# Kernel optimization log

Measured on AMD Instinct MI355X. Metric: run time of the kernel, lower is better.

Reference implementation:

```python
import jax, jax.numpy as jnp
import numpy as np

NQ = 14
DIM = 2 ** NQ


def make_unitary(M):
    # QR-based unitarization, matching torch: Q * (diag(R)/|diag(R)|) broadcast over rows
    Q, R = jnp.linalg.qr(M)
    d = jnp.diagonal(R, axis1=-2, axis2=-1)
    ph = d / jnp.abs(d)
    return Q * ph[..., None, :]


def apply_1q(state, U, q, nq):
    # state: [B] + [2]*nq, qubit q lives at axis 1 + (nq-1-q) (qubit 0 = LSB)
    ax = 1 + (nq - 1 - q)
    s = jnp.moveaxis(state, ax, 1)
    shp = s.shape
    s = s.reshape(shp[0], 2, -1)
    s = jnp.einsum('ji,bir->bjr', U, s)
    return jnp.moveaxis(s.reshape(shp), 1, ax)


def apply_1q_batched(state, U, q, nq):
    # U: [B,2,2] per-batch gate
    ax = 1 + (nq - 1 - q)
    s = jnp.moveaxis(state, ax, 1)
    shp = s.shape
    s = s.reshape(shp[0], 2, -1)
    s = jnp.einsum('bji,bir->bjr', U, s)
    return jnp.moveaxis(s.reshape(shp), 1, ax)


def apply_2q(state, U4, qa, qb, nq):
    # source: gate index = bit_qa + 2*bit_qb, so reshape(4,4)->(2,2,2,2) gives [ob,oa,ib,ia]
    G = U4.reshape(2, 2, 2, 2)
    ax_a = 1 + (nq - 1 - qa)
    ax_b = 1 + (nq - 1 - qb)
    s = jnp.moveaxis(state, (ax_b, ax_a), (1, 2))
    shp = s.shape
    s = s.reshape(shp[0], 2, 2, -1)
    s = jnp.einsum('JKjk,bjkr->bJKr', G, s)
    return jnp.moveaxis(s.reshape(shp), (1, 2), (ax_b, ax_a))


def setup_inputs() -> dict:
    key = jax.random.key(0)
    ks = jax.random.split(key, 9)
    B, H = 256, 1024
    return {
        'x': jax.random.normal(ks[0], (B, H), dtype=jnp.float32),
        'w_pre': jax.random.normal(ks[1], (2 * NQ, H), dtype=jnp.float32) * 0.03,
        'b_pre': jax.random.normal(ks[2], (2 * NQ,), dtype=jnp.float32) * 0.01,
        'w_post': jax.random.normal(ks[3], (H, DIM), dtype=jnp.float32) * 0.01,
        'b_post': jax.random.normal(ks[4], (H,), dtype=jnp.float32) * 0.01,
        'sq_re': jax.random.normal(ks[5], (NQ, 2, 2), dtype=jnp.float32),
        'sq_im': jax.random.normal(ks[6], (NQ, 2, 2), dtype=jnp.float32),
        'ent_re': jax.random.normal(ks[7], (NQ - 1, 4, 4), dtype=jnp.float32),
        'ent_im': jax.random.normal(ks[8], (NQ - 1, 4, 4), dtype=jnp.float32),
    }


def reference(x, w_pre, b_pre, w_post, b_post, sq_re, sq_im, ent_re, ent_im):
    B = x.shape[0]
    nq = NQ
    # pre_quantum Linear
    params = x @ w_pre.T + b_pre  # [B, 2*nq]
    theta = params[:, 0::2]
    phi = params[:, 1::2]
    c = jnp.cos(theta / 2)
    s = jnp.sin(theta / 2)
    # initial state = rotation gates applied to |0...0>: keep only column 0 of each gate
    v = jnp.stack([c.astype(jnp.complex64), (jnp.exp(1j * phi) * s).astype(jnp.complex64)], axis=-1)  # [B,nq,2]
    state = v[:, nq - 1]  # MSB axis first (qubit nq-1)
    for q in range(nq - 2, -1, -1):
        state = (state[:, :, None] * v[:, q][:, None, :]).reshape(B, -1)
    state = state.reshape((B,) + (2,) * nq)
    # learned unitaries (batched QR over gate index)
    sq = make_unitary(sq_re.astype(jnp.complex64) + 1j * sq_im.astype(jnp.complex64))
    ent = make_unitary(ent_re.astype(jnp.complex64) + 1j * ent_im.astype(jnp.complex64))
    for q in range(nq):
        state = apply_1q(state, sq[q], q, nq)
    for q in range(nq - 1):
        state = apply_2q(state, ent[q], q, q + 1, nq)
    amp = state.reshape(B, -1)  # C-order flatten => index = sum(bit_q << q), matches source
    probs = amp.real ** 2 + amp.imag ** 2  # [B, dim]
    return probs @ w_post.T + b_post  # [B, hidden]
```

## Files before the change

### kernel.cpp

```cpp
#include <hip/hip_runtime.h>
#include <hip/hip_bf16.h>
#include <math.h>

#define NQ 14
#define DIM 16384
#define NB 256
#define NH 1024
#define SPLITK 16
#define KCHUNK (DIM / SPLITK)
#define BK 64

typedef __attribute__((ext_vector_type(8))) short bf16x8;
typedef __attribute__((ext_vector_type(4))) float f32x4;

#define SW(i) ((i) + 5 * ((i) >> 5))
#define SW_SIZE (DIM + 5 * (DIM / 32))

__global__ __launch_bounds__(256) void k_pre(const float* __restrict__ x,
                                             const float* __restrict__ w_pre,
                                             const float* __restrict__ b_pre,
                                             float* __restrict__ v_buf) {
    int b = blockIdx.x;
    int t = threadIdx.x;
    __shared__ float red[28][4];

    float4 xs = ((const float4*)(x + (size_t)b * NH))[t];
    float acc[28];
#pragma unroll
    for (int j = 0; j < 28; j++) {
        float4 w = ((const float4*)(w_pre + (size_t)j * NH))[t];
        acc[j] = xs.x * w.x + xs.y * w.y + xs.z * w.z + xs.w * w.w;
    }
    int lane = t & 63, wv = t >> 6;
#pragma unroll
    for (int j = 0; j < 28; j++) {
        float a = acc[j];
#pragma unroll
        for (int o = 32; o > 0; o >>= 1) a += __shfl_down(a, o);
        if (lane == 0) red[j][wv] = a;
    }
    __syncthreads();
    if (t < NQ) {
        float p0 = red[2*t][0] + red[2*t][1] + red[2*t][2] + red[2*t][3] + b_pre[2*t];
        float p1 = red[2*t+1][0] + red[2*t+1][1] + red[2*t+1][2] + red[2*t+1][3] + b_pre[2*t+1];
        float c = cosf(p0 * 0.5f), s = sinf(p0 * 0.5f);
        float cp = cosf(p1), sp = sinf(p1);
        ((float4*)v_buf)[b * NQ + t] = make_float4(c, 0.f, cp * s, sp * s);
    }
}

template <int N>
__device__ void gs_qr(const float* Mre, const float* Mim, float* Uout) {
    double qre[N][N], qim[N][N];
#pragma unroll
    for (int j = 0; j < N; j++) {
        double vr[N], vi[N];
#pragma unroll
        for (int r = 0; r < N; r++) { vr[r] = (double)Mre[r * N + j]; vi[r] = (double)Mim[r * N + j]; }
#pragma unroll
        for (int i = 0; i < N; i++) {
            if (i < j) {
                double rr = 0.0, ri = 0.0;
#pragma unroll
                for (int r = 0; r < N; r++) {
                    rr += qre[i][r] * vr[r] + qim[i][r] * vi[r];
                    ri += qre[i][r] * vi[r] - qim[i][r] * vr[r];
                }
#pragma unroll
                for (int r = 0; r < N; r++) {
                    vr[r] -= rr * qre[i][r] - ri * qim[i][r];
                    vi[r] -= rr * qim[i][r] + ri * qre[i][r];
                }
            }
        }
        double nn = 0.0;
#pragma unroll
        for (int r = 0; r < N; r++) nn += vr[r] * vr[r] + vi[r] * vi[r];
        double inv = 1.0 / sqrt(nn);
#pragma unroll
        for (int r = 0; r < N; r++) { qre[j][r] = vr[r] * inv; qim[j][r] = vi[r] * inv; }
    }
#pragma unroll
    for (int r = 0; r < N; r++)
#pragma unroll
        for (int j = 0; j < N; j++) {
            Uout[(r * N + j) * 2]     = (float)qre[j][r];
            Uout[(r * N + j) * 2 + 1] = (float)qim[j][r];
        }
}

__global__ void k_qr(const float* __restrict__ sq_re, const float* __restrict__ sq_im,
                     const float* __restrict__ ent_re, const float* __restrict__ ent_im,
                     float* __restrict__ sqU, float* __restrict__ entU) {
    int t = threadIdx.x;
    if (t < NQ) {
        gs_qr<2>(sq_re + t * 4, sq_im + t * 4, sqU + t * 8);
    } else if (t < NQ + (NQ - 1)) {
        int e = t - NQ;
        gs_qr<4>(ent_re + e * 16, ent_im + e * 16, entU + e * 32);
    }
}

extern __shared__ float smem[];
__global__ __launch_bounds__(1024) void k_state(const float* __restrict__ v_buf,
                                                const float* __restrict__ sqU,
                                                const float* __restrict__ entU,
                                                __hip_bfloat16* __restrict__ probs) {
    const int b = blockIdx.x, t = threadIdx.x;
    float* sre  = smem;
    float* simg = smem + SW_SIZE;
    float* wloc = smem + 2 * SW_SIZE;
    float* g2   = wloc + NQ * 4;
    float* hi   = g2 + (NQ - 1) * 32;

    if (t < (NQ - 1) * 32) g2[t] = entU[t];
    if (t < NQ) {
        float4 v = ((const float4*)v_buf)[b * NQ + t];
        const float* u = sqU + t * 8;
        float w0r = u[0]*v.x - u[1]*v.y + u[2]*v.z - u[3]*v.w;
        float w0i = u[0]*v.y + u[1]*v.x + u[2]*v.w + u[3]*v.z;
        float w1r = u[4]*v.x - u[5]*v.y + u[6]*v.z - u[7]*v.w;
        float w1i = u[4]*v.y + u[5]*v.x + u[6]*v.w + u[7]*v.z;
        wloc[t*4+0] = w0r; wloc[t*4+1] = w0i; wloc[t*4+2] = w1r; wloc[t*4+3] = w1i;
    }
    __syncthreads();
    if (t < 16) {
        float hr = 1.f, hii = 0.f;
#pragma unroll
        for (int q = 10; q < 14; q++) {
            int bit = (t >> (q - 10)) & 1;
            float br = wloc[q*4 + 2*bit], bi = wloc[q*4 + 2*bit + 1];
            float nr = hr*br - hii*bi, ni = hr*bi + hii*br;
            hr = nr; hii = ni;
        }
        hi[2*t] = hr; hi[2*t+1] = hii;
    }
    __syncthreads();
    {
        float lr = 1.f, li = 0.f;
#pragma unroll
        for (int q = 0; q < 10; q++) {
            int bit = (t >> q) & 1;
            float br = wloc[q*4 + 2*bit], bi = wloc[q*4 + 2*bit + 1];
            float nr = lr*br - li*bi, ni = lr*bi + li*br;
            lr = nr; li = ni;
        }
#pragma unroll
        for (int k = 0; k < 16; k++) {
            int idx = k * 1024 + t;
            float hr = hi[2*k], hii = hi[2*k+1];
            sre[SW(idx)]  = lr*hr - li*hii;
            simg[SW(idx)] = lr*hii + li*hr;
        }
    }
    __syncthreads();

    for (int e = 0; e < NQ - 1; e++) {
        float gr[4][4], gi[4][4];
#pragma unroll
        for (int m = 0; m < 16; m++) {
            gr[m >> 2][m & 3] = g2[e*32 + 2*m];
            gi[m >> 2][m & 3] = g2[e*32 + 2*m + 1];
        }
        const int q = e, mask = (1 << q) - 1;
#pragma unroll
        for (int k = 0; k < 4; k++) {
            int g = k * 1024 + t;
            int base = ((g & ~mask) << 2) | (g & mask);
            int ia[4];
#pragma unroll
            for (int m = 0; m < 4; m++) ia[m] = SW(base + (m << q));
            float ar[4], ai[4];
#pragma unroll
            for (int m = 0; m < 4; m++) { ar[m] = sre[ia[m]]; ai[m] = simg[ia[m]]; }
            float orr[4], oii[4];
#pragma unroll
            for (int r = 0; r < 4; r++) {
                float nr = 0.f, ni = 0.f;
#pragma unroll
                for (int c = 0; c < 4; c++) {
                    nr += gr[r][c] * ar[c] - gi[r][c] * ai[c];
                    ni += gr[r][c] * ai[c] + gi[r][c] * ar[c];
                }
                orr[r] = nr; oii[r] = ni;
            }
#pragma unroll
            for (int r = 0; r < 4; r++) { sre[ia[r]] = orr[r]; simg[ia[r]] = oii[r]; }
        }
        __syncthreads();
    }

#pragma unroll
    for (int k = 0; k < 16; k++) {
        int idx = k * 1024 + t;
        float r = sre[SW(idx)], i2 = simg[SW(idx)];
        probs[(size_t)b * DIM + idx] = __float2bfloat16(r * r + i2 * i2);
    }
}

__global__ __launch_bounds__(512) void k_gemm_mfma(const ushort* __restrict__ A,
                                                   const float* __restrict__ Bw,
                                                   float* __restrict__ part) {
    __shared__ ushort As[128 * 64];
    __shared__ ushort Bs[128 * 64];
    const int t = threadIdx.x;
    const int l = t & 63, wid = t >> 6;
    const int wr = wid >> 2, wc = wid & 3;
    const int bm0 = blockIdx.x * 128;
    const int hn0 = blockIdx.y * 128;
    const int k0  = blockIdx.z * KCHUNK;

    f32x4 acc[4][2];
#pragma unroll
    for (int m = 0; m < 4; m++)
#pragma unroll
        for (int n = 0; n < 2; n++) acc[m][n] = (f32x4){0.f, 0.f, 0.f, 0.f};

    const int srow = t >> 3;
    const int scol = (t & 7) * 8;
    const int alr  = l >> 3;
    const int alc  = (l & 7) * 8;

    for (int kc = 0; kc < KCHUNK; kc += BK) {
        const int kbase = k0 + kc;
#pragma unroll
        for (int i = 0; i < 2; i++) {
            const int r0 = i * 64 + wid * 8;
            const ushort* gsrc = A + (size_t)(bm0 + r0 + alr) * DIM + kbase + alc;
            __builtin_amdgcn_global_load_lds(
                (const __attribute__((address_space(1))) unsigned int*)gsrc,
                (__attribute__((address_space(3))) unsigned int*)&As[r0 * 64],
                16, 0, 0);
        }
#pragma unroll
        for (int i = 0; i < 2; i++) {
            const int r = i * 64 + srow;
            const float* bsrc = Bw + (size_t)(hn0 + r) * DIM + kbase + scol;
            float4 b0 = *(const float4*)(bsrc);
            float4 b1 = *(const float4*)(bsrc + 4);
            union { ushort u[8]; bf16x8 v; } pk;
            __hip_bfloat16 h;
            h = __float2bfloat16(b0.x); pk.u[0] = *(ushort*)&h;
            h = __float2bfloat16(b0.y); pk.u[1] = *(ushort*)&h;
            h = __float2bfloat16(b0.z); pk.u[2] = *(ushort*)&h;
            h = __float2bfloat16(b0.w); pk.u[3] = *(ushort*)&h;
            h = __float2bfloat16(b1.x); pk.u[4] = *(ushort*)&h;
            h = __float2bfloat16(b1.y); pk.u[5] = *(ushort*)&h;
            h = __float2bfloat16(b1.z); pk.u[6] = *(ushort*)&h;
            h = __float2bfloat16(b1.w); pk.u[7] = *(ushort*)&h;
            *(bf16x8*)&Bs[r * 64 + scol] = pk.v;
        }
        __syncthreads();
#pragma unroll
        for (int kk = 0; kk < 2; kk++) {
            const int kcol = kk * 32 + (l >> 4) * 8;
            bf16x8 a[4], b[2];
#pragma unroll
            for (int m = 0; m < 4; m++)
                a[m] = *(const bf16x8*)&As[(wr * 64 + m * 16 + (l & 15)) * 64 + kcol];
#pragma unroll
            for (int n = 0; n < 2; n++)
                b[n] = *(const bf16x8*)&Bs[(wc * 32 + n * 16 + (l & 15)) * 64 + kcol];
#pragma unroll
            for (int m = 0; m < 4; m++)
#pragma unroll
                for (int n = 0; n < 2; n++)
                    acc[m][n] = __builtin_amdgcn_mfma_f32_16x16x32_bf16(
                        a[m], b[n], acc[m][n], 0, 0, 0);
        }
        __syncthreads();
    }
    float* dst = part + (size_t)blockIdx.z * (NB * NH);
#pragma unroll
    for (int m = 0; m < 4; m++) {
        const int row = bm0 + wr * 64 + m * 16 + (l >> 4) * 4;
#pragma unroll
        for (int n = 0; n < 2; n++) {
            const int col = hn0 + wc * 32 + n * 16 + (l & 15);
#pragma unroll
            for (int j = 0; j < 4; j++)
                dst[(size_t)(row + j) * NH + col] = acc[m][n][j];
        }
    }
}

__global__ __launch_bounds__(256) void k_reduce(const float* __restrict__ part,
                                                const float* __restrict__ b_post,
                                                float* __restrict__ out) {
    int i = blockIdx.x * 256 + threadIdx.x;
    float s = b_post[i & (NH - 1)];
#pragma unroll
    for (int z = 0; z < SPLITK; z++) s += part[(size_t)z * (NB * NH) + i];
    out[i] = s;
}

extern "C" void kernel_launch(void* const* d_in, const int* in_sizes, int n_in,
                              void* d_out, int out_size, void* d_ws, size_t ws_size,
                              hipStream_t stream) {
    const float* x      = (const float*)d_in[0];
    const float* w_pre  = (const float*)d_in[1];
    const float* b_pre  = (const float*)d_in[2];
    const float* w_post = (const float*)d_in[3];
    const float* b_post = (const float*)d_in[4];
    const float* sq_re  = (const float*)d_in[5];
    const float* sq_im  = (const float*)d_in[6];
    const float* ent_re = (const float*)d_in[7];
    const float* ent_im = (const float*)d_in[8];
    float* out = (float*)d_out;
    char* ws   = (char*)d_ws;

    float* v_buf         = (float*)(ws);
    float* sqU           = (float*)(ws + 57344);
    float* entU          = (float*)(ws + 57792);
    __hip_bfloat16* probs = (__hip_bfloat16*)(ws + 59456);
    float* part          = (float*)(ws + 8448064);

    k_pre<<<NB, 256, 0, stream>>>(x, w_pre, b_pre, v_buf);
    k_qr<<<1, 64, 0, stream>>>(sq_re, sq_im, ent_re, ent_im, sqU, entU);

    const int smem_bytes = (2 * SW_SIZE + NQ * 4 + (NQ - 1) * 32 + 32) * 4;
    (void)hipFuncSetAttribute((const void*)k_state,
                              hipFuncAttributeMaxDynamicSharedMemorySize, smem_bytes);
    k_state<<<NB, 1024, smem_bytes, stream>>>(v_buf, sqU, entU, probs);

    k_gemm_mfma<<<dim3(2, 8, SPLITK), 512, 0, stream>>>((const ushort*)probs, w_post, part);
    k_reduce<<<(NB * NH) / 256, 256, 0, stream>>>(part, b_post, out);
}
```

Measured before the change: 206.5 us.

## Register-resident gate chain with shared-memory transposes, fuse QR into pre kernel, smaller GEMM tiles

The state kernel now keeps 16 amplitudes per thread in registers and applies three 2-qubit gates locally between shared-memory transposes. This replaces a per-gate shared-memory round trip plus barrier for each of the 13 gates. The QR kernel launch is folded into extra blocks of the pre kernel to save one launch. The GEMM switches to 64x64 tiles with 256 threads, giving more blocks for occupancy at the cost of lower per-block data reuse.

```diff
diff --git a/kernel.cpp b/kernel.cpp
--- a/kernel.cpp
+++ b/kernel.cpp
@@ -16,12 +16,66 @@
 #define SW(i) ((i) + 5 * ((i) >> 5))
 #define SW_SIZE (DIM + 5 * (DIM / 32))
 
+template <int N>
+__device__ void gs_qr(const float* Mre, const float* Mim, float* Uout) {
+    double qre[N][N], qim[N][N];
+#pragma unroll
+    for (int j = 0; j < N; j++) {
+        double vr[N], vi[N];
+#pragma unroll
+        for (int r = 0; r < N; r++) { vr[r] = (double)Mre[r * N + j]; vi[r] = (double)Mim[r * N + j]; }
+#pragma unroll
+        for (int i = 0; i < N; i++) {
+            if (i < j) {
+                double rr = 0.0, ri = 0.0;
+#pragma unroll
+                for (int r = 0; r < N; r++) {
+                    rr += qre[i][r] * vr[r] + qim[i][r] * vi[r];
+                    ri += qre[i][r] * vi[r] - qim[i][r] * vr[r];
+                }
+#pragma unroll
+                for (int r = 0; r < N; r++) {
+                    vr[r] -= rr * qre[i][r] - ri * qim[i][r];
+                    vi[r] -= rr * qim[i][r] + ri * qre[i][r];
+                }
+            }
+        }
+        double nn = 0.0;
+#pragma unroll
+        for (int r = 0; r < N; r++) nn += vr[r] * vr[r] + vi[r] * vi[r];
+        double inv = 1.0 / sqrt(nn);
+#pragma unroll
+        for (int r = 0; r < N; r++) { qre[j][r] = vr[r] * inv; qim[j][r] = vi[r] * inv; }
+    }
+#pragma unroll
+    for (int r = 0; r < N; r++)
+#pragma unroll
+        for (int j = 0; j < N; j++) {
+            Uout[(r * N + j) * 2]     = (float)qre[j][r];
+            Uout[(r * N + j) * 2 + 1] = (float)qim[j][r];
+        }
+}
+
 __global__ __launch_bounds__(256) void k_pre(const float* __restrict__ x,
                                              const float* __restrict__ w_pre,
                                              const float* __restrict__ b_pre,
-                                             float* __restrict__ v_buf) {
-    int b = blockIdx.x;
-    int t = threadIdx.x;
+                                             const float* __restrict__ sq_re,
+                                             const float* __restrict__ sq_im,
+                                             const float* __restrict__ ent_re,
+                                             const float* __restrict__ ent_im,
+                                             float* __restrict__ v_buf,
+                                             float* __restrict__ sqU,
+                                             float* __restrict__ entU) {
+    const int b = blockIdx.x;
+    const int t = threadIdx.x;
+    if (b >= NB) {
+        if (b == NB) {
+            if (t < NQ) gs_qr<2>(sq_re + t * 4, sq_im + t * 4, sqU + t * 8);
+        } else {
+            if (t < NQ - 1) gs_qr<4>(ent_re + t * 16, ent_im + t * 16, entU + t * 32);
+        }
+        return;
+    }
     __shared__ float red[28][4];
 
     float4 xs = ((const float4*)(x + (size_t)b * NH))[t];
@@ -49,57 +103,48 @@
     }
 }
 
-template <int N>
-__device__ void gs_qr(const float* Mre, const float* Mim, float* Uout) {
-    double qre[N][N], qim[N][N];
-#pragma unroll
-    for (int j = 0; j < N; j++) {
-        double vr[N], vi[N];
-#pragma unroll
-        for (int r = 0; r < N; r++) { vr[r] = (double)Mre[r * N + j]; vi[r] = (double)Mim[r * N + j]; }
-#pragma unroll
-        for (int i = 0; i < N; i++) {
-            if (i < j) {
-                double rr = 0.0, ri = 0.0;
-#pragma unroll
-                for (int r = 0; r < N; r++) {
-                    rr += qre[i][r] * vr[r] + qim[i][r] * vi[r];
-                    ri += qre[i][r] * vi[r] - qim[i][r] * vr[r];
-                }
-#pragma unroll
-                for (int r = 0; r < N; r++) {
-                    vr[r] -= rr * qre[i][r] - ri * qim[i][r];
-                    vi[r] -= rr * qim[i][r] + ri * qre[i][r];
-                }
-            }
-        }
-        double nn = 0.0;
-#pragma unroll
-        for (int r = 0; r < N; r++) nn += vr[r] * vr[r] + vi[r] * vi[r];
-        double inv = 1.0 / sqrt(nn);
-#pragma unroll
-        for (int r = 0; r < N; r++) { qre[j][r] = vr[r] * inv; qim[j][r] = vi[r] * inv; }
-    }
-#pragma unroll
-    for (int r = 0; r < N; r++)
-#pragma unroll
-        for (int j = 0; j < N; j++) {
-            Uout[(r * N + j) * 2]     = (float)qre[j][r];
-            Uout[(r * N + j) * 2 + 1] = (float)qim[j][r];
-        }
-}
-
-__global__ void k_qr(const float* __restrict__ sq_re, const float* __restrict__ sq_im,
-                     const float* __restrict__ ent_re, const float* __restrict__ ent_im,
-                     float* __restrict__ sqU, float* __restrict__ entU) {
-    int t = threadIdx.x;
-    if (t < NQ) {
-        gs_qr<2>(sq_re + t * 4, sq_im + t * 4, sqU + t * 8);
-    } else if (t < NQ + (NQ - 1)) {
-        int e = t - NQ;
-        gs_qr<4>(ent_re + e * 16, ent_im + e * 16, entU + e * 32);
-    }
-}
+#define APPLY_GATE(I, GP) do {                                                \
+    float gr_[16], gi_[16];                                                   \
+    _Pragma("unroll")                                                         \
+    for (int m_ = 0; m_ < 16; m_++) { gr_[m_] = (GP)[2*m_]; gi_[m_] = (GP)[2*m_+1]; } \
+    _Pragma("unroll")                                                         \
+    for (int g_ = 0; g_ < 4; g_++) {                                          \
+        const int base_ = (I)==0 ? (g_<<2) : ((I)==1 ? ((g_&1)|((g_>>1)<<3)) : g_); \
+        float xr_[4], xi_[4];                                                 \
+        _Pragma("unroll")                                                     \
+        for (int c_ = 0; c_ < 4; c_++) { xr_[c_] = ar[base_+(c_<<(I))]; xi_[c_] = ai[base_+(c_<<(I))]; } \
+        _Pragma("unroll")                                                     \
+        for (int r_ = 0; r_ < 4; r_++) {                                      \
+            float nr_ = 0.f, ni_ = 0.f;                                       \
+            _Pragma("unroll")                                                 \
+            for (int c_ = 0; c_ < 4; c_++) {                                  \
+                nr_ += gr_[r_*4+c_]*xr_[c_] - gi_[r_*4+c_]*xi_[c_];           \
+                ni_ += gr_[r_*4+c_]*xi_[c_] + gi_[r_*4+c_]*xr_[c_];           \
+            }                                                                 \
+            ar[base_+(r_<<(I))] = nr_; ai[base_+(r_<<(I))] = ni_;             \
+        }                                                                     \
+    }                                                                         \
+} while (0)
+
+#define IDX_W0(r) (((t) << 4) | (r))
+#define IDX_W1(r) (((t) & 7) | ((r) << 3) | (((t) >> 3) << 7))
+#define IDX_W2(r) (((t) & 63) | ((r) << 6) | (((t) >> 6) << 10))
+#define IDX_W3(r) (((t) & 511) | ((r) << 9) | (((t) >> 9) << 13))
+#define IDX_W4(r) ((t) | ((r) << 10))
+
+#define TRANSPOSE(IDX_OLD, IDX_NEW) do {                                      \
+    _Pragma("unroll")                                                         \
+    for (int r_ = 0; r_ < 16; r_++) {                                         \
+        int o_ = SW(IDX_OLD(r_));                                             \
+        sre[o_] = ar[r_]; simg[o_] = ai[r_];                                  \
+    }                                                                         \
+    __syncthreads();                                                          \
+    _Pragma("unroll")                                                         \
+    for (int r_ = 0; r_ < 16; r_++) {                                         \
+        int n_ = SW(IDX_NEW(r_));                                             \
+        ar[r_] = sre[n_]; ai[r_] = simg[n_];                                  \
+    }                                                                         \
+} while (0)
 
 extern __shared__ float smem[];
 __global__ __launch_bounds__(1024) void k_state(const float* __restrict__ v_buf,
@@ -111,7 +156,6 @@
     float* simg = smem + SW_SIZE;
     float* wloc = smem + 2 * SW_SIZE;
     float* g2   = wloc + NQ * 4;
-    float* hi   = g2 + (NQ - 1) * 32;
 
     if (t < (NQ - 1) * 32) g2[t] = entU[t];
     if (t < NQ) {
@@ -124,95 +168,81 @@
         wloc[t*4+0] = w0r; wloc[t*4+1] = w0i; wloc[t*4+2] = w1r; wloc[t*4+3] = w1i;
     }
     __syncthreads();
-    if (t < 16) {
-        float hr = 1.f, hii = 0.f;
-#pragma unroll
-        for (int q = 10; q < 14; q++) {
-            int bit = (t >> (q - 10)) & 1;
+
+    float ar[16], ai[16];
+    {
+        float cr = 1.f, ci = 0.f;
+#pragma unroll
+        for (int q = 4; q < 14; q++) {
+            int bit = (t >> (q - 4)) & 1;
             float br = wloc[q*4 + 2*bit], bi = wloc[q*4 + 2*bit + 1];
-            float nr = hr*br - hii*bi, ni = hr*bi + hii*br;
-            hr = nr; hii = ni;
-        }
-        hi[2*t] = hr; hi[2*t+1] = hii;
-    }
-    __syncthreads();
-    {
-        float lr = 1.f, li = 0.f;
-#pragma unroll
-        for (int q = 0; q < 10; q++) {
-            int bit = (t >> q) & 1;
-            float br = wloc[q*4 + 2*bit], bi = wloc[q*4 + 2*bit + 1];
-            float nr = lr*br - li*bi, ni = lr*bi + li*br;
-            lr = nr; li = ni;
-        }
-#pragma unroll
-        for (int k = 0; k < 16; k++) {
-            int idx = k * 1024 + t;
-            float hr = hi[2*k], hii = hi[2*k+1];
-            sre[SW(idx)]  = lr*hr - li*hii;
-            simg[SW(idx)] = lr*hii + li*hr;
-        }
-    }
-    __syncthreads();
-
-    for (int e = 0; e < NQ - 1; e++) {
-        float gr[4][4], gi[4][4];
-#pragma unroll
-        for (int m = 0; m < 16; m++) {
-            gr[m >> 2][m & 3] = g2[e*32 + 2*m];
-            gi[m >> 2][m & 3] = g2[e*32 + 2*m + 1];
-        }
-        const int q = e, mask = (1 << q) - 1;
-#pragma unroll
-        for (int k = 0; k < 4; k++) {
-            int g = k * 1024 + t;
-            int base = ((g & ~mask) << 2) | (g & mask);
-            int ia[4];
-#pragma unroll
-            for (int m = 0; m < 4; m++) ia[m] = SW(base + (m << q));
-            float ar[4], ai[4];
-#pragma unroll
-            for (int m = 0; m < 4; m++) { ar[m] = sre[ia[m]]; ai[m] = simg[ia[m]]; }
-            float orr[4], oii[4];
-#pragma unroll
-            for (int r = 0; r < 4; r++) {
-                float nr = 0.f, ni = 0.f;
-#pragma unroll
-                for (int c = 0; c < 4; c++) {
-                    nr += gr[r][c] * ar[c] - gi[r][c] * ai[c];
-                    ni += gr[r][c] * ai[c] + gi[r][c] * ar[c];
-                }
-                orr[r] = nr; oii[r] = ni;
-            }
-#pragma unroll
-            for (int r = 0; r < 4; r++) { sre[ia[r]] = orr[r]; simg[ia[r]] = oii[r]; }
-        }
-        __syncthreads();
-    }
-
-#pragma unroll
-    for (int k = 0; k < 16; k++) {
-        int idx = k * 1024 + t;
-        float r = sre[SW(idx)], i2 = simg[SW(idx)];
-        probs[(size_t)b * DIM + idx] = __float2bfloat16(r * r + i2 * i2);
-    }
-}
-
-__global__ __launch_bounds__(512) void k_gemm_mfma(const ushort* __restrict__ A,
+            float nr = cr*br - ci*bi, ni = cr*bi + ci*br;
+            cr = nr; ci = ni;
+        }
+        float p01r[4], p01i[4], p23r[4], p23i[4];
+#pragma unroll
+        for (int j = 0; j < 4; j++) {
+            int b0 = j & 1, b1 = j >> 1;
+            float a0r = wloc[0*4 + 2*b0], a0i = wloc[0*4 + 2*b0 + 1];
+            float a1r = wloc[1*4 + 2*b1], a1i = wloc[1*4 + 2*b1 + 1];
+            p01r[j] = a0r*a1r - a0i*a1i; p01i[j] = a0r*a1i + a0i*a1r;
+            float a2r = wloc[2*4 + 2*b0], a2i = wloc[2*4 + 2*b0 + 1];
+            float a3r = wloc[3*4 + 2*b1], a3i = wloc[3*4 + 2*b1 + 1];
+            p23r[j] = a2r*a3r - a2i*a3i; p23i[j] = a2r*a3i + a2i*a3r;
+        }
+#pragma unroll
+        for (int r = 0; r < 16; r++) {
+            int lo = r & 3, hi2 = r >> 2;
+            float tr = cr*p01r[lo] - ci*p01i[lo];
+            float ti = cr*p01i[lo] + ci*p01r[lo];
+            ar[r] = tr*p23r[hi2] - ti*p23i[hi2];
+            ai[r] = tr*p23i[hi2] + ti*p23r[hi2];
+        }
+    }
+
+    APPLY_GATE(0, g2 + 0*32);
+    APPLY_GATE(1, g2 + 1*32);
+    APPLY_GATE(2, g2 + 2*32);
+    TRANSPOSE(IDX_W0, IDX_W1);
+    APPLY_GATE(0, g2 + 3*32);
+    APPLY_GATE(1, g2 + 4*32);
+    APPLY_GATE(2, g2 + 5*32);
+    __syncthreads();
+    TRANSPOSE(IDX_W1, IDX_W2);
+    APPLY_GATE(0, g2 + 6*32);
+    APPLY_GATE(1, g2 + 7*32);
+    APPLY_GATE(2, g2 + 8*32);
+    __syncthreads();
+    TRANSPOSE(IDX_W2, IDX_W3);
+    APPLY_GATE(0, g2 + 9*32);
+    APPLY_GATE(1, g2 + 10*32);
+    APPLY_GATE(2, g2 + 11*32);
+    __syncthreads();
+    TRANSPOSE(IDX_W3, IDX_W4);
+    APPLY_GATE(2, g2 + 12*32);
+
+#pragma unroll
+    for (int r = 0; r < 16; r++) {
+        float pr = ar[r]*ar[r] + ai[r]*ai[r];
+        probs[(size_t)b * DIM + (r << 10) + t] = __float2bfloat16(pr);
+    }
+}
+
+__global__ __launch_bounds__(256) void k_gemm_mfma(const ushort* __restrict__ A,
                                                    const float* __restrict__ Bw,
                                                    float* __restrict__ part) {
-    __shared__ ushort As[128 * 64];
-    __shared__ ushort Bs[128 * 64];
+    __shared__ ushort As[64 * 64];
+    __shared__ ushort Bs[64 * 64];
     const int t = threadIdx.x;
     const int l = t & 63, wid = t >> 6;
-    const int wr = wid >> 2, wc = wid & 3;
-    const int bm0 = blockIdx.x * 128;
-    const int hn0 = blockIdx.y * 128;
+    const int wr = wid >> 1, wc = wid & 1;
+    const int bm0 = blockIdx.x * 64;
+    const int hn0 = blockIdx.y * 64;
     const int k0  = blockIdx.z * KCHUNK;
 
-    f32x4 acc[4][2];
-#pragma unroll
-    for (int m = 0; m < 4; m++)
+    f32x4 acc[2][2];
+#pragma unroll
+    for (int m = 0; m < 2; m++)
 #pragma unroll
         for (int n = 0; n < 2; n++) acc[m][n] = (f32x4){0.f, 0.f, 0.f, 0.f};
 
@@ -225,7 +255,7 @@
         const int kbase = k0 + kc;
 #pragma unroll
         for (int i = 0; i < 2; i++) {
-            const int r0 = i * 64 + wid * 8;
+            const int r0 = (i * 4 + wid) * 8;
             const ushort* gsrc = A + (size_t)(bm0 + r0 + alr) * DIM + kbase + alc;
             __builtin_amdgcn_global_load_lds(
                 (const __attribute__((address_space(1))) unsigned int*)gsrc,
@@ -234,7 +264,7 @@
         }
 #pragma unroll
         for (int i = 0; i < 2; i++) {
-            const int r = i * 64 + srow;
+            const int r = i * 32 + srow;
             const float* bsrc = Bw + (size_t)(hn0 + r) * DIM + kbase + scol;
             float4 b0 = *(const float4*)(bsrc);
             float4 b1 = *(const float4*)(bsrc + 4);
@@ -254,26 +284,26 @@
 #pragma unroll
         for (int kk = 0; kk < 2; kk++) {
             const int kcol = kk * 32 + (l >> 4) * 8;
-            bf16x8 a[4], b[2];
-#pragma unroll
-            for (int m = 0; m < 4; m++)
-                a[m] = *(const bf16x8*)&As[(wr * 64 + m * 16 + (l & 15)) * 64 + kcol];
+            bf16x8 a[2], bb[2];
+#pragma unroll
+            for (int m = 0; m < 2; m++)
+                a[m] = *(const bf16x8*)&As[(wr * 32 + m * 16 + (l & 15)) * 64 + kcol];
 #pragma unroll
             for (int n = 0; n < 2; n++)
-                b[n] = *(const bf16x8*)&Bs[(wc * 32 + n * 16 + (l & 15)) * 64 + kcol];
-#pragma unroll
-            for (int m = 0; m < 4; m++)
+                bb[n] = *(const bf16x8*)&Bs[(wc * 32 + n * 16 + (l & 15)) * 64 + kcol];
+#pragma unroll
+            for (int m = 0; m < 2; m++)
 #pragma unroll
                 for (int n = 0; n < 2; n++)
                     acc[m][n] = __builtin_amdgcn_mfma_f32_16x16x32_bf16(
-                        a[m], b[n], acc[m][n], 0, 0, 0);
+                        a[m], bb[n], acc[m][n], 0, 0, 0);
         }
         __syncthreads();
     }
     float* dst = part + (size_t)blockIdx.z * (NB * NH);
 #pragma unroll
-    for (int m = 0; m < 4; m++) {
-        const int row = bm0 + wr * 64 + m * 16 + (l >> 4) * 4;
+    for (int m = 0; m < 2; m++) {
+        const int row = bm0 + wr * 32 + m * 16 + (l >> 4) * 4;
 #pragma unroll
         for (int n = 0; n < 2; n++) {
             const int col = hn0 + wc * 32 + n * 16 + (l & 15);
@@ -309,20 +339,20 @@
     float* out = (float*)d_out;
     char* ws   = (char*)d_ws;
 
-    float* v_buf         = (float*)(ws);
-    float* sqU           = (float*)(ws + 57344);
-    float* entU          = (float*)(ws + 57792);
+    float* v_buf          = (float*)(ws);
+    float* sqU            = (float*)(ws + 57344);
+    float* entU           = (float*)(ws + 57792);
     __hip_bfloat16* probs = (__hip_bfloat16*)(ws + 59456);
-    float* part          = (float*)(ws + 8448064);
-
-    k_pre<<<NB, 256, 0, stream>>>(x, w_pre, b_pre, v_buf);
-    k_qr<<<1, 64, 0, stream>>>(sq_re, sq_im, ent_re, ent_im, sqU, entU);
-
-    const int smem_bytes = (2 * SW_SIZE + NQ * 4 + (NQ - 1) * 32 + 32) * 4;
+    float* part           = (float*)(ws + 8448064);
+
+    k_pre<<<NB + 2, 256, 0, stream>>>(x, w_pre, b_pre, sq_re, sq_im, ent_re, ent_im,
+                                      v_buf, sqU, entU);
+
+    const int smem_bytes = (2 * SW_SIZE + NQ * 4 + (NQ - 1) * 32) * 4;
     (void)hipFuncSetAttribute((const void*)k_state,
                               hipFuncAttributeMaxDynamicSharedMemorySize, smem_bytes);
     k_state<<<NB, 1024, smem_bytes, stream>>>(v_buf, sqU, entU, probs);
 
-    k_gemm_mfma<<<dim3(2, 8, SPLITK), 512, 0, stream>>>((const ushort*)probs, w_post, part);
+    k_gemm_mfma<<<dim3(4, 16, SPLITK), 256, 0, stream>>>((const ushort*)probs, w_post, part);
     k_reduce<<<(NB * NH) / 256, 256, 0, stream>>>(part, b_post, out);
 }
```

Measured after the change: 265.4 us. 1.29x slower.
